# Kernel optimization log

Measured on AMD Instinct MI355X. Metric: run time of the kernel, lower is better.

Reference implementation:

```python
import jax, jax.numpy as jnp
import numpy as np

V = 32000   # vocab_size
H = 256     # hidden_dim
HALF = H // 2
B = 64
L = 2048
LN_EPS = 1e-5
DELTA_EPS = 1e-6


def setup_inputs() -> dict:
    key = jax.random.key(0)
    ks = jax.random.split(key, 8)
    s = 0.02
    return {
        "seq": jax.random.randint(ks[0], (B, L), 0, V),
        # Encoder params
        "embed": jax.random.normal(ks[1], (V, H), jnp.float32) * s,
        "W1": jax.random.normal(ks[2], (H, 2 * H), jnp.float32) * s,
        "b1": jnp.zeros((2 * H,), jnp.float32),
        "W2": jax.random.normal(ks[3], (2 * H, H), jnp.float32) * s,
        "b2": jnp.zeros((H,), jnp.float32),
        "gamma": jnp.ones((H,), jnp.float32),
        "beta": jnp.zeros((H,), jnp.float32),
        # sem_p: Linear(H, HALF)
        "Wp": jax.random.normal(ks[4], (H, HALF), jnp.float32) * s,
        "bp": jnp.zeros((HALF,), jnp.float32),
        # out: Linear(HALF, V)
        "Wo": jax.random.normal(ks[5], (HALF, V), jnp.float32) * s,
        "bo": jnp.zeros((V,), jnp.float32),
    }


def reference(seq, embed, W1, b1, W2, b2, gamma, beta, Wp, bp, Wo, bo):
    # Encoder: embed -> FFN -> residual -> LayerNorm
    e = embed[seq]                                      # [B, L, H]
    f = jnp.maximum(e @ W1 + b1, 0.0) @ W2 + b2         # [B, L, H]
    x = e + f
    mu = jnp.mean(x, axis=-1, keepdims=True)
    var = jnp.mean((x - mu) ** 2, axis=-1, keepdims=True)
    h = (x - mu) / jnp.sqrt(var + LN_EPS) * gamma + beta  # [B, L, H]

    # Project all timesteps once (sem_p applied to h[:, t] and the last query)
    p = h @ Wp + bp                                     # [B, L, HALF]

    # Delta-rule recurrent state update over t = 0 .. L-2
    ks_seq = jnp.swapaxes(p[:, :-1, :], 0, 1)           # [L-1, B, HALF]

    def step(M, k):
        vps = jnp.einsum('bij,bj->bi', M, k)            # read
        dvs = k - vps / (jnp.sum(k * k, axis=-1, keepdims=True) + DELTA_EPS)
        M = M + dvs[:, :, None] * k[:, None, :]         # rank-1 write
        return M, None

    M0 = jnp.zeros((B, HALF, HALF), h.dtype)
    M_s, _ = jax.lax.scan(step, M0, ks_seq)

    # Read with projected last-position query
    cs = jnp.einsum('bij,bj->bi', M_s, p[:, -1, :])     # [B, HALF]
    return cs @ Wo + bo                                 # [B, V]
```

## Files before the change

### kernel.cpp

```cpp
#include <hip/hip_runtime.h>

#define Vv 32000
#define Ll 2048

typedef __bf16 bf16x8 __attribute__((ext_vector_type(8)));
typedef float  f32x4  __attribute__((ext_vector_type(4)));

__device__ __forceinline__ unsigned short f2bf(float f) {
    unsigned u = __builtin_bit_cast(unsigned, f);
    u += 0x7fffu + ((u >> 16) & 1u);
    return (unsigned short)(u >> 16);
}
__device__ __forceinline__ float bf2f(unsigned short s) {
    unsigned u = (unsigned)s << 16;
    return __builtin_bit_cast(float, u);
}
__device__ __forceinline__ void unpk8(uint4 v, float* o) {
    o[0] = bf2f((unsigned short)(v.x & 0xffff)); o[1] = bf2f((unsigned short)(v.x >> 16));
    o[2] = bf2f((unsigned short)(v.y & 0xffff)); o[3] = bf2f((unsigned short)(v.y >> 16));
    o[4] = bf2f((unsigned short)(v.z & 0xffff)); o[5] = bf2f((unsigned short)(v.z >> 16));
    o[6] = bf2f((unsigned short)(v.w & 0xffff)); o[7] = bf2f((unsigned short)(v.w >> 16));
}

#define MFMA(a, b, c) __builtin_amdgcn_mfma_f32_16x16x32_bf16(a, b, c, 0, 0, 0)
#define GLL16(gsrc, ldst)                                                    \
    __builtin_amdgcn_global_load_lds(                                        \
        (const __attribute__((address_space(1))) void*)(gsrc),               \
        (__attribute__((address_space(3))) void*)(ldst), 16, 0, 0)
#define GLL4(gsrc, ldst)                                                     \
    __builtin_amdgcn_global_load_lds(                                        \
        (const __attribute__((address_space(1))) void*)(gsrc),               \
        (__attribute__((address_space(3))) void*)(ldst), 4, 0, 0)

__global__ __launch_bounds__(256) void prep_kernel(
    const float* __restrict__ W1, const float* __restrict__ W2,
    const float* __restrict__ Wp, unsigned short* __restrict__ W1T,
    unsigned short* __restrict__ W2T, unsigned short* __restrict__ WpT,
    float* __restrict__ zrow)
{
    int idx = blockIdx.x * 256 + threadIdx.x;
    if (blockIdx.x == 575 && threadIdx.x < 64) zrow[threadIdx.x] = 0.f;
    if (idx < 65536) {
        int e0 = idx * 2, n = e0 >> 8, k = e0 & 255;
        unsigned lo = f2bf(W1[(size_t)k * 512 + n]);
        unsigned hi = f2bf(W1[(size_t)(k + 1) * 512 + n]);
        ((unsigned*)W1T)[idx] = lo | (hi << 16);
    } else if (idx < 131072) {
        int i = idx - 65536, e0 = i * 2, n = e0 >> 9, k = e0 & 511;
        unsigned lo = f2bf(W2[(size_t)k * 256 + n]);
        unsigned hi = f2bf(W2[(size_t)(k + 1) * 256 + n]);
        ((unsigned*)W2T)[i] = lo | (hi << 16);
    } else {
        int i = idx - 131072, e0 = i * 2, n = e0 >> 8, k = e0 & 255;
        unsigned lo = f2bf(Wp[(size_t)k * 128 + n]);
        unsigned hi = f2bf(Wp[(size_t)(k + 1) * 128 + n]);
        ((unsigned*)WpT)[i] = lo | (hi << 16);
    }
}

__global__ __launch_bounds__(256) void embconv_kernel(
    const float* __restrict__ embed, unsigned short* __restrict__ embbf)
{
    int idx = blockIdx.x * 256 + threadIdx.x;
    const float4 a = ((const float4*)embed)[(size_t)idx * 2];
    const float4 b = ((const float4*)embed)[(size_t)idx * 2 + 1];
    uint4 pk;
    pk.x = (unsigned)f2bf(a.x) | ((unsigned)f2bf(a.y) << 16);
    pk.y = (unsigned)f2bf(a.z) | ((unsigned)f2bf(a.w) << 16);
    pk.z = (unsigned)f2bf(b.x) | ((unsigned)f2bf(b.y) << 16);
    pk.w = (unsigned)f2bf(b.z) | ((unsigned)f2bf(b.w) << 16);
    ((uint4*)embbf)[idx] = pk;
}

__global__ __launch_bounds__(512, 4) void enc_kernel(
    const unsigned short* __restrict__ embbf,
    const unsigned short* __restrict__ W1T, const float* __restrict__ b1,
    const unsigned short* __restrict__ W2T, const float* __restrict__ b2,
    const float* __restrict__ gamma, const float* __restrict__ beta,
    const unsigned short* __restrict__ WpT, const float* __restrict__ bp,
    unsigned short* __restrict__ ptab)
{
    __shared__ char sE[32 * 512];
    __shared__ char sU[32 * 1024];
    __shared__ float sPart[32][8][2];
    __shared__ float sMR[32][2];

    const int tid  = threadIdx.x;
    const int lane = tid & 63;
    const int w    = tid >> 6;
    const int l15  = lane & 15;
    const int lk   = lane >> 4;
    const int n0   = blockIdx.x * 32;
    const int swl  = (l15 & 7) << 4;

    #pragma unroll
    for (int cc = 0; cc < 2; ++cc) {
        int c = cc * 512 + tid;
        int row  = c >> 5;
        int slot = (c & 31) << 4;
        int kbs  = slot ^ ((row & 7) << 4);
        GLL16((const char*)embbf + (size_t)(n0 + row) * 512 + kbs,
              sE + (cc * 512 + (tid & 448)) * 16);
    }
    __syncthreads();

    #pragma unroll
    for (int nf2 = 0; nf2 < 2; ++nf2) {
        f32x4 acc1[2][2];
        acc1[0][0] = acc1[0][1] = acc1[1][0] = acc1[1][1] = (f32x4){0.f, 0.f, 0.f, 0.f};
        const char* w1p = (const char*)W1T + (size_t)(w * 64 + nf2 * 32 + l15) * 512 + lk * 16;
        bf16x8 bfr[16];
        #pragma unroll
        for (int ks = 0; ks < 8; ++ks) {
            bfr[ks * 2]     = *(const bf16x8*)(w1p + ks * 64);
            bfr[ks * 2 + 1] = *(const bf16x8*)(w1p + 16 * 512 + ks * 64);
        }
        #pragma unroll
        for (int ks = 0; ks < 8; ++ks) {
            int ka = (ks * 64 + lk * 16) ^ swl;
            bf16x8 a0 = *(const bf16x8*)(sE + l15 * 512 + ka);
            bf16x8 a1 = *(const bf16x8*)(sE + (16 + l15) * 512 + ka);
            acc1[0][0] = MFMA(a0, bfr[ks * 2],     acc1[0][0]);
            acc1[1][0] = MFMA(a1, bfr[ks * 2],     acc1[1][0]);
            acc1[0][1] = MFMA(a0, bfr[ks * 2 + 1], acc1[0][1]);
            acc1[1][1] = MFMA(a1, bfr[ks * 2 + 1], acc1[1][1]);
        }
        float bv0 = b1[w * 64 + nf2 * 32 + l15];
        float bv1 = b1[w * 64 + nf2 * 32 + 16 + l15];
        #pragma unroll
        for (int mi = 0; mi < 2; ++mi)
            #pragma unroll
            for (int nj = 0; nj < 2; ++nj) {
                float bv = nj ? bv1 : bv0;
                #pragma unroll
                for (int r = 0; r < 4; ++r) {
                    int row = mi * 16 + lk * 4 + r;
                    int col = w * 64 + nf2 * 32 + nj * 16 + l15;
                    float v = fmaxf(acc1[mi][nj][r] + bv, 0.f);
                    *(unsigned short*)(sU + row * 1024 + ((col * 2) ^ ((row & 7) << 4))) = f2bf(v);
                }
            }
    }
    __syncthreads();

    f32x4 acc2[2][2];
    acc2[0][0] = acc2[0][1] = acc2[1][0] = acc2[1][1] = (f32x4){0.f, 0.f, 0.f, 0.f};
    {
        const char* w2p = (const char*)W2T + (size_t)(w * 32 + l15) * 1024 + lk * 16;
        #pragma unroll
        for (int h = 0; h < 2; ++h) {
            bf16x8 bfr[16];
            #pragma unroll
            for (int ks = 0; ks < 8; ++ks) {
                int kss = h * 8 + ks;
                bfr[ks * 2]     = *(const bf16x8*)(w2p + kss * 64);
                bfr[ks * 2 + 1] = *(const bf16x8*)(w2p + 16 * 1024 + kss * 64);
            }
            #pragma unroll
            for (int ks = 0; ks < 8; ++ks) {
                int kss = h * 8 + ks;
                int ka = (kss * 64 + lk * 16) ^ swl;
                bf16x8 a0 = *(const bf16x8*)(sU + l15 * 1024 + ka);
                bf16x8 a1 = *(const bf16x8*)(sU + (16 + l15) * 1024 + ka);
                acc2[0][0] = MFMA(a0, bfr[ks * 2],     acc2[0][0]);
                acc2[1][0] = MFMA(a1, bfr[ks * 2],     acc2[1][0]);
                acc2[0][1] = MFMA(a0, bfr[ks * 2 + 1], acc2[0][1]);
                acc2[1][1] = MFMA(a1, bfr[ks * 2 + 1], acc2[1][1]);
            }
        }
    }

    float b2v[2], gv[2], btv[2];
    #pragma unroll
    for (int nj = 0; nj < 2; ++nj) {
        int col = w * 32 + nj * 16 + l15;
        b2v[nj] = b2[col]; gv[nj] = gamma[col]; btv[nj] = beta[col];
    }
    #pragma unroll
    for (int mi = 0; mi < 2; ++mi)
        #pragma unroll
        for (int r = 0; r < 4; ++r) {
            int row = mi * 16 + lk * 4 + r;
            int swr = (row & 7) << 4;
            float s1 = 0.f, s2 = 0.f;
            #pragma unroll
            for (int nj = 0; nj < 2; ++nj) {
                int col = w * 32 + nj * 16 + l15;
                float e = bf2f(*(const unsigned short*)(sE + row * 512 + ((col * 2) ^ swr)));
                float x = acc2[mi][nj][r] + b2v[nj] + e;
                acc2[mi][nj][r] = x;
                s1 += x; s2 = fmaf(x, x, s2);
            }
            s1 += __shfl_xor(s1, 1); s2 += __shfl_xor(s2, 1);
            s1 += __shfl_xor(s1, 2); s2 += __shfl_xor(s2, 2);
            s1 += __shfl_xor(s1, 4); s2 += __shfl_xor(s2, 4);
            s1 += __shfl_xor(s1, 8); s2 += __shfl_xor(s2, 8);
            if (l15 == 0) { sPart[row][w][0] = s1; sPart[row][w][1] = s2; }
        }
    __syncthreads();
    if (tid < 32) {
        float t1 = 0.f, t2 = 0.f;
        #pragma unroll
        for (int ww = 0; ww < 8; ++ww) { t1 += sPart[tid][ww][0]; t2 += sPart[tid][ww][1]; }
        float mu  = t1 * (1.f / 256.f);
        float var = t2 * (1.f / 256.f) - mu * mu;
        sMR[tid][0] = mu;
        sMR[tid][1] = rsqrtf(var + 1e-5f);
    }
    __syncthreads();
    #pragma unroll
    for (int mi = 0; mi < 2; ++mi)
        #pragma unroll
        for (int r = 0; r < 4; ++r) {
            int row = mi * 16 + lk * 4 + r;
            int swr = (row & 7) << 4;
            float mu = sMR[row][0], rs = sMR[row][1];
            #pragma unroll
            for (int nj = 0; nj < 2; ++nj) {
                int col = w * 32 + nj * 16 + l15;
                float h = (acc2[mi][nj][r] - mu) * rs * gv[nj] + btv[nj];
                *(unsigned short*)(sE + row * 512 + ((col * 2) ^ swr)) = f2bf(h);
            }
        }
    __syncthreads();

    f32x4 acc3[2];
    acc3[0] = acc3[1] = (f32x4){0.f, 0.f, 0.f, 0.f};
    {
        const char* wpp = (const char*)WpT + (size_t)(w * 16 + l15) * 512 + lk * 16;
        bf16x8 bfr[8];
        #pragma unroll
        for (int ks = 0; ks < 8; ++ks)
            bfr[ks] = *(const bf16x8*)(wpp + ks * 64);
        #pragma unroll
        for (int ks = 0; ks < 8; ++ks) {
            int ka = (ks * 64 + lk * 16) ^ swl;
            bf16x8 a0 = *(const bf16x8*)(sE + l15 * 512 + ka);
            bf16x8 a1 = *(const bf16x8*)(sE + (16 + l15) * 512 + ka);
            acc3[0] = MFMA(a0, bfr[ks], acc3[0]);
            acc3[1] = MFMA(a1, bfr[ks], acc3[1]);
        }
    }
    {
        float bpv = bp[w * 16 + l15];
        #pragma unroll
        for (int mi = 0; mi < 2; ++mi)
            #pragma unroll
            for (int r = 0; r < 4; ++r) {
                int row = mi * 16 + lk * 4 + r;
                int col = w * 16 + l15;
                *(unsigned short*)(sU + row * 256 + col * 2) = f2bf(acc3[mi][r] + bpv);
            }
    }
    __syncthreads();
    {
        int row = tid >> 4, slot = (tid & 15) << 4;
        *(uint4*)((char*)ptab + (size_t)(n0 + row) * 256 + slot) =
            *(const uint4*)(sU + row * 256 + slot);
    }
}

__global__ __launch_bounds__(256) void sprep_kernel(
    const int* __restrict__ seq, const unsigned short* __restrict__ ptab,
    char* __restrict__ SBg)
{
    __shared__ unsigned short sK[64 * 136];
    __shared__ float sG[10 * 16 * 17];
    __shared__ float sM[4 * 16 * 17];
    __shared__ float sQ[64];
    __shared__ float sW[64 * 132];

    const int blk  = blockIdx.x;
    const int b    = blk >> 5, ch = blk & 31;
    const int t_hi = 2047 - (ch << 6);
    const int tid  = threadIdx.x;
    const int lane = tid & 63;
    const int wv   = tid >> 6;
    const int l15  = lane & 15, lk = lane >> 4;

    #pragma unroll
    for (int i = 0; i < 4; ++i) {
        int c = i * 256 + tid;
        int row = c >> 4, j = c & 15;
        int t = t_hi - row;
        if (t == 2047) {
            *(uint4*)((char*)sK + row * 272 + j * 16) = (uint4){0u, 0u, 0u, 0u};
        } else {
            int v = seq[b * 2048 + t];
            *(uint4*)((char*)sK + row * 272 + j * 16) =
                *(const uint4*)((const char*)(ptab + (size_t)v * 128) + j * 16);
        }
    }
    __syncthreads();

    {
        int q = 0;
        #pragma unroll
        for (int ti = 0; ti < 4; ++ti)
            #pragma unroll
            for (int tj = 0; tj <= ti; ++tj, ++q) {
                if ((q & 3) != wv) continue;
                f32x4 acc = (f32x4){0.f, 0.f, 0.f, 0.f};
                #pragma unroll
                for (int ks = 0; ks < 4; ++ks) {
                    bf16x8 fa = *(const bf16x8*)((const char*)sK + (ti * 16 + l15) * 272 + ks * 64 + lk * 16);
                    bf16x8 fb = *(const bf16x8*)((const char*)sK + (tj * 16 + l15) * 272 + ks * 64 + lk * 16);
                    acc = MFMA(fa, fb, acc);
                }
                #pragma unroll
                for (int r = 0; r < 4; ++r)
                    sG[q * 272 + (lk * 4 + r) * 17 + l15] = acc[r];
            }
    }
    __syncthreads();

    if (tid < 64) {
        int dq = (lk * (lk + 3)) >> 1;
        float d = sG[dq * 272 + l15 * 17 + l15] + 1e-6f;
        sQ[tid] = 1.0f / d;
    }
    __syncthreads();

    if (tid < 64) {
        const int g = lk, c = l15;
        const float* Tg = &sG[((g * (g + 3)) >> 1) * 272];
        float qv[16], av[16], mcol[16];
        #pragma unroll
        for (int r = 0; r < 16; ++r) { qv[r] = sQ[g * 16 + r]; av[r] = 0.f; }
        #pragma unroll
        for (int r = 0; r < 16; ++r) {
            float mr = (((r == c) ? 1.f : 0.f) - av[r]) * qv[r];
            mcol[r] = mr;
            #pragma unroll
            for (int i = r + 1; i < 16; ++i)
                av[i] = fmaf(Tg[i * 17 + r], mr, av[i]);
        }
        #pragma unroll
        for (int r = 0; r < 16; ++r)
            sM[g * 272 + r * 17 + c] = mcol[r];
    }
    __syncthreads();

    const int rr = tid & 15, dq8 = tid >> 4;
    #pragma unroll 1
    for (int s = 0; s < 4; ++s) {
        float a[8];
        {
            uint4 kv = *(const uint4*)((const char*)sK + (16 * s + rr) * 272 + dq8 * 16);
            unpk8(kv, a);
        }
        #pragma unroll
        for (int j = 0; j < 3; ++j) {
            if (j >= s) break;
            const float* Tb = &sG[(((s * (s + 1)) >> 1) + j) * 272];
            #pragma unroll
            for (int m = 0; m < 16; ++m) {
                float t = Tb[rr * 17 + m];
                const float* wrow = &sW[(16 * j + m) * 132 + dq8 * 8];
                f32x4 w0 = *(const f32x4*)(wrow);
                f32x4 w1 = *(const f32x4*)(wrow + 4);
                a[0] = fmaf(-t, w0.x, a[0]); a[1] = fmaf(-t, w0.y, a[1]);
                a[2] = fmaf(-t, w0.z, a[2]); a[3] = fmaf(-t, w0.w, a[3]);
                a[4] = fmaf(-t, w1.x, a[4]); a[5] = fmaf(-t, w1.y, a[5]);
                a[6] = fmaf(-t, w1.z, a[6]); a[7] = fmaf(-t, w1.w, a[7]);
            }
        }
        {
            float* wrow = &sW[(16 * s + rr) * 132 + dq8 * 8];
            *(f32x4*)(wrow)     = (f32x4){a[0], a[1], a[2], a[3]};
            *(f32x4*)(wrow + 4) = (f32x4){a[4], a[5], a[6], a[7]};
        }
        __syncthreads();
        float o[8];
        #pragma unroll
        for (int v = 0; v < 8; ++v) o[v] = 0.f;
        #pragma unroll
        for (int cc = 0; cc < 16; ++cc) {
            float mm = sM[s * 272 + rr * 17 + cc];
            const float* wrow = &sW[(16 * s + cc) * 132 + dq8 * 8];
            f32x4 w0 = *(const f32x4*)(wrow);
            f32x4 w1 = *(const f32x4*)(wrow + 4);
            o[0] = fmaf(mm, w0.x, o[0]); o[1] = fmaf(mm, w0.y, o[1]);
            o[2] = fmaf(mm, w0.z, o[2]); o[3] = fmaf(mm, w0.w, o[3]);
            o[4] = fmaf(mm, w1.x, o[4]); o[5] = fmaf(mm, w1.y, o[5]);
            o[6] = fmaf(mm, w1.z, o[6]); o[7] = fmaf(mm, w1.w, o[7]);
        }
        __syncthreads();
        {
            float* wrow = &sW[(16 * s + rr) * 132 + dq8 * 8];
            *(f32x4*)(wrow)     = (f32x4){o[0], o[1], o[2], o[3]};
            *(f32x4*)(wrow + 4) = (f32x4){o[4], o[5], o[6], o[7]};
        }
        __syncthreads();
    }

    char* blob = SBg + (size_t)blk * 17408;
    unsigned* wtp = (unsigned*)blob;
    {
        int i = tid & 63;
        #pragma unroll
        for (int dg = 0; dg < 16; ++dg) {
            int d2 = (tid >> 6) * 16 + dg;
            float2 wvp = *(const float2*)&sW[i * 132 + d2 * 2];
            wtp[d2 * 64 + i] = (unsigned)f2bf(wvp.x) | ((unsigned)f2bf(wvp.y) << 16);
        }
    }
    if (tid < 64) {
        int dq = (lk * (lk + 3)) >> 1;
        float d = sG[dq * 272 + l15 * 17 + l15] + 1e-6f;
        *(float*)(blob + 16384 + tid * 4) = d;
    }
}

__global__ __launch_bounds__(512) void scan_kernel(
    const int* __restrict__ seq, const unsigned short* __restrict__ ptab,
    const char* __restrict__ SBg, const float* __restrict__ zrow,
    float* __restrict__ csb)
{
    __shared__ int sSeq[2048];
    __shared__ unsigned short sKb[2][8192];
    __shared__ __align__(16) char sBlob[2][16640];
    __shared__ float  sPZ[8][64];
    __shared__ float2 sPC[8][64];

    const int b    = blockIdx.x;
    const int tid  = threadIdx.x;
    const int lane = tid & 63;
    const int w    = tid >> 6;

    *(int4*)&sSeq[tid * 4] = *(const int4*)&seq[b * 2048 + tid * 4];
    float u0, u1;
    {
        int vq = seq[b * 2048 + 2047];
        unsigned pk = *(const unsigned*)(ptab + (size_t)vq * 128 + lane * 2);
        u0 = bf2f((unsigned short)(pk & 0xffff));
        u1 = bf2f((unsigned short)(pk >> 16));
    }
    float csv0 = 0.f, csv1 = 0.f;
    __syncthreads();

    auto STAGE = [&](int s, int ch) {
        int t_hi = 2047 - (ch << 6);
        #pragma unroll
        for (int kk = 0; kk < 2; ++kk) {
            int k = w * 2 + kk;
            int g = k * 64 + lane;
            int r = g >> 4, sd = g & 15;
            int t = t_hi - r;
            int v = sSeq[t];
            const char* srow = (t == 2047) ? (const char*)zrow
                                           : (const char*)(ptab + (size_t)v * 128);
            GLL16(srow + sd * 16, (char*)sKb[s] + k * 1024);
        }
        const char* bsrc = SBg + ((size_t)b * 32 + ch) * 17408;
        #pragma unroll
        for (int kk = 0; kk < 2; ++kk) {
            int k = w * 2 + kk;
            GLL16(bsrc + k * 1024 + lane * 16, (char*)sBlob[s] + k * 1024);
        }
        if (w == 7)
            GLL4(bsrc + 16384 + lane * 4, (char*)sBlob[s] + 16384);
    };

    STAGE(0, 0); STAGE(1, 1);

    #pragma unroll 1
    for (int c = 0; c < 32; ++c) {
        const int cur = c & 1;
        if (c < 31) {
            if (w == 7) asm volatile("s_waitcnt vmcnt(5)" ::: "memory");
            else        asm volatile("s_waitcnt vmcnt(4)" ::: "memory");
        } else {
            asm volatile("s_waitcnt vmcnt(0)" ::: "memory");
        }
        __builtin_amdgcn_s_barrier();
        __builtin_amdgcn_sched_barrier(0);

        const unsigned short* kb = sKb[cur];
        const unsigned* wt = (const unsigned*)(sBlob[cur]);
        const float* dgv = (const float*)(sBlob[cur] + 16384);

        float zp = 0.f;
        #pragma unroll
        for (int j = 0; j < 8; ++j) {
            int d2 = w * 8 + j;
            unsigned wp = wt[d2 * 64 + lane];
            float ua = __shfl(u0, d2);
            float ub = __shfl(u1, d2);
            zp = fmaf(bf2f((unsigned short)(wp & 0xffff)), ua, zp);
            zp = fmaf(bf2f((unsigned short)(wp >> 16)),    ub, zp);
        }
        sPZ[w][lane] = zp;
        asm volatile("s_waitcnt lgkmcnt(0)" ::: "memory");
        __builtin_amdgcn_s_barrier();
        __builtin_amdgcn_sched_barrier(0);

        float z = 0.f;
        #pragma unroll
        for (int ww = 0; ww < 8; ++ww) z += sPZ[ww][lane];
        float ci = z * dgv[lane];

        float du0 = 0.f, du1 = 0.f;
        #pragma unroll
        for (int j = 0; j < 8; ++j) {
            int i = w * 8 + j;
            float zi  = __shfl(z, i);
            float cii = __shfl(ci, i);
            unsigned kp = *(const unsigned*)((const char*)kb + i * 256 + lane * 4);
            float k0 = bf2f((unsigned short)(kp & 0xffff));
            float k1 = bf2f((unsigned short)(kp >> 16));
            du0  = fmaf(zi,  k0, du0);  du1  = fmaf(zi,  k1, du1);
            csv0 = fmaf(cii, k0, csv0); csv1 = fmaf(cii, k1, csv1);
        }
        sPC[w][lane] = make_float2(du0, du1);
        asm volatile("s_waitcnt lgkmcnt(0)" ::: "memory");
        __builtin_amdgcn_s_barrier();
        __builtin_amdgcn_sched_barrier(0);

        if (c + 2 < 32) STAGE(cur, c + 2);

        float s0 = 0.f, s1 = 0.f;
        #pragma unroll
        for (int ww = 0; ww < 8; ++ww) {
            float2 p = sPC[ww][lane];
            s0 += p.x; s1 += p.y;
        }
        u0 -= s0; u1 -= s1;
    }

    asm volatile("s_waitcnt lgkmcnt(0)" ::: "memory");
    __builtin_amdgcn_s_barrier();
    sPC[w][lane] = make_float2(csv0, csv1);
    asm volatile("s_waitcnt lgkmcnt(0)" ::: "memory");
    __builtin_amdgcn_s_barrier();
    if (w == 0) {
        float a0 = 0.f, a1 = 0.f;
        #pragma unroll
        for (int ww = 0; ww < 8; ++ww) {
            float2 p = sPC[ww][lane];
            a0 += p.x; a1 += p.y;
        }
        csb[b * 128 + lane * 2]     = a0;
        csb[b * 128 + lane * 2 + 1] = a1;
    }
}

__global__ __launch_bounds__(256) void out_kernel(
    const float* __restrict__ cs, const float* __restrict__ Wo,
    const float* __restrict__ bo, float* __restrict__ out)
{
    __shared__ float sC[64 * 128];
    const int tid = threadIdx.x;
    #pragma unroll
    for (int r = 0; r < 8; ++r)
        ((float4*)sC)[r * 256 + tid] = ((const float4*)cs)[r * 256 + tid];
    __syncthreads();

    const int j  = blockIdx.x * 64 + (tid & 63);
    const int rg = tid >> 6;
    float acc[16];
    #pragma unroll
    for (int r = 0; r < 16; ++r) acc[r] = 0.f;
    for (int k0 = 0; k0 < 128; k0 += 4) {
        float w0 = Wo[(size_t)(k0 + 0) * Vv + j];
        float w1 = Wo[(size_t)(k0 + 1) * Vv + j];
        float w2 = Wo[(size_t)(k0 + 2) * Vv + j];
        float w3 = Wo[(size_t)(k0 + 3) * Vv + j];
        #pragma unroll
        for (int r = 0; r < 16; ++r) {
            float4 c = *(const float4*)&sC[(rg * 16 + r) * 128 + k0];
            acc[r] = fmaf(c.x, w0, fmaf(c.y, w1, fmaf(c.z, w2, fmaf(c.w, w3, acc[r]))));
        }
    }
    float bj = bo[j];
    #pragma unroll
    for (int r = 0; r < 16; ++r)
        out[(size_t)(rg * 16 + r) * Vv + j] = acc[r] + bj;
}

extern "C" void kernel_launch(void* const* d_in, const int* in_sizes, int n_in,
                              void* d_out, int out_size, void* d_ws, size_t ws_size,
                              hipStream_t stream)
{
    const int*   seq   = (const int*)  d_in[0];
    const float* embed = (const float*)d_in[1];
    const float* W1    = (const float*)d_in[2];
    const float* b1    = (const float*)d_in[3];
    const float* W2    = (const float*)d_in[4];
    const float* b2    = (const float*)d_in[5];
    const float* gamma = (const float*)d_in[6];
    const float* beta  = (const float*)d_in[7];
    const float* Wp    = (const float*)d_in[8];
    const float* bp    = (const float*)d_in[9];
    const float* Wo    = (const float*)d_in[10];
    const float* bo    = (const float*)d_in[11];
    float* out = (float*)d_out;

    char* wsb = (char*)d_ws;
    unsigned short* ptab  = (unsigned short*)(wsb);
    char*           SBg   = wsb + 8192000;
    unsigned short* W1T   = (unsigned short*)(wsb + 43843584);
    unsigned short* W2T   = (unsigned short*)(wsb + 44105728);
    unsigned short* WpT   = (unsigned short*)(wsb + 44367872);
    float*          csb   = (float*)(wsb + 44433408);
    float*          zrow  = (float*)(wsb + 44466176);
    unsigned short* embbf = (unsigned short*)(wsb + 44466432);

    prep_kernel<<<576, 256, 0, stream>>>(W1, W2, Wp, W1T, W2T, WpT, zrow);
    embconv_kernel<<<4000, 256, 0, stream>>>(embed, embbf);
    enc_kernel<<<Vv / 32, 512, 0, stream>>>(embbf, W1T, b1, W2T, b2,
                                            gamma, beta, WpT, bp, ptab);
    sprep_kernel<<<2048, 256, 0, stream>>>(seq, ptab, SBg);
    scan_kernel<<<64, 512, 0, stream>>>(seq, ptab, SBg, zrow, csb);
    out_kernel<<<Vv / 64, 256, 0, stream>>>(csb, Wo, bo, out);
}
```

Measured before the change: 211.0 us.

## Split encoder into tiled FFN1 kernel and LDS-pipelined FFN2/projection kernel

The fused encoder kernel becomes two kernels. encA computes the first FFN layer with ReLU on 128x128 tiles, staging both the embeddings and W1 in shared memory, and writes the hidden activations to a global buffer. encB reloads those activations and streams W2 through a double-buffered shared-memory pipeline with explicit waitcnt and barriers. It also stages Wp in shared memory instead of loading it straight into registers. The aim is better weight reuse and less redundant global weight traffic per block, at the cost of a 32 MB intermediate write and read and one extra launch.

New measurement: 205.8 us. -2.5%, faster.

```diff
diff --git a/kernel.cpp b/kernel.cpp
--- a/kernel.cpp
+++ b/kernel.cpp
@@ -72,16 +72,95 @@
     ((uint4*)embbf)[idx] = pk;
 }
 
-__global__ __launch_bounds__(512, 4) void enc_kernel(
+__global__ __launch_bounds__(512, 2) void encA_kernel(
     const unsigned short* __restrict__ embbf,
     const unsigned short* __restrict__ W1T, const float* __restrict__ b1,
-    const unsigned short* __restrict__ W2T, const float* __restrict__ b2,
+    unsigned short* __restrict__ Ug)
+{
+    __shared__ char sA[65536];
+    __shared__ char sB[65536];
+
+    const int tid  = threadIdx.x;
+    const int lane = tid & 63;
+    const int w    = tid >> 6;
+    const int rh   = w >> 2;
+    const int cq   = w & 3;
+    const int l15  = lane & 15;
+    const int lk   = lane >> 4;
+    const int n0   = (blockIdx.x >> 2) * 128;
+    const int c0   = (blockIdx.x & 3) * 128;
+    const int swl  = (l15 & 7) << 4;
+
+    #pragma unroll
+    for (int i = 0; i < 8; ++i) {
+        int id = i * 512 + tid;
+        int row = id >> 5, slot = (id & 31) << 4;
+        GLL16((const char*)embbf + (size_t)(n0 + row) * 512 + (slot ^ ((row & 7) << 4)),
+              sA + (size_t)(i * 512 + (tid & 448)) * 16);
+    }
+    #pragma unroll
+    for (int i = 0; i < 8; ++i) {
+        int id = i * 512 + tid;
+        int col = id >> 5, slot = (id & 31) << 4;
+        GLL16((const char*)W1T + (size_t)(c0 + col) * 512 + (slot ^ ((col & 7) << 4)),
+              sB + (size_t)(i * 512 + (tid & 448)) * 16);
+    }
+    __syncthreads();
+
+    f32x4 acc[4][2];
+    #pragma unroll
+    for (int m = 0; m < 4; ++m)
+        #pragma unroll
+        for (int n = 0; n < 2; ++n) acc[m][n] = (f32x4){0.f, 0.f, 0.f, 0.f};
+    #pragma unroll
+    for (int ks = 0; ks < 8; ++ks) {
+        int ka = (ks * 64 + lk * 16) ^ swl;
+        bf16x8 b0 = *(const bf16x8*)(sB + (cq * 32 + l15) * 512 + ka);
+        bf16x8 b1v = *(const bf16x8*)(sB + (cq * 32 + 16 + l15) * 512 + ka);
+        #pragma unroll
+        for (int mi = 0; mi < 4; ++mi) {
+            bf16x8 a = *(const bf16x8*)(sA + (rh * 64 + mi * 16 + l15) * 512 + ka);
+            acc[mi][0] = MFMA(a, b0,  acc[mi][0]);
+            acc[mi][1] = MFMA(a, b1v, acc[mi][1]);
+        }
+    }
+
+    float bv0 = b1[c0 + cq * 32 + l15];
+    float bv1 = b1[c0 + cq * 32 + 16 + l15];
+    __syncthreads();
+    #pragma unroll
+    for (int mi = 0; mi < 4; ++mi)
+        #pragma unroll
+        for (int nj = 0; nj < 2; ++nj) {
+            float bv = nj ? bv1 : bv0;
+            #pragma unroll
+            for (int r = 0; r < 4; ++r) {
+                int row = rh * 64 + mi * 16 + lk * 4 + r;
+                int col = cq * 32 + nj * 16 + l15;
+                *(unsigned short*)(sA + row * 256 + col * 2) =
+                    f2bf(fmaxf(acc[mi][nj][r] + bv, 0.f));
+            }
+        }
+    __syncthreads();
+    #pragma unroll
+    for (int i = 0; i < 4; ++i) {
+        int id = i * 512 + tid;
+        int row = id >> 4, slot = (id & 15) << 4;
+        *(uint4*)((char*)Ug + (size_t)(n0 + row) * 1024 + c0 * 2 + slot) =
+            *(const uint4*)(sA + row * 256 + slot);
+    }
+}
+
+__global__ __launch_bounds__(512, 2) void encB_kernel(
+    const unsigned short* __restrict__ embbf, const unsigned short* __restrict__ Ug,
+    const char* __restrict__ W2Tc, const float* __restrict__ b2,
     const float* __restrict__ gamma, const float* __restrict__ beta,
     const unsigned short* __restrict__ WpT, const float* __restrict__ bp,
     unsigned short* __restrict__ ptab)
 {
     __shared__ char sE[32 * 512];
     __shared__ char sU[32 * 1024];
+    __shared__ char sWB[65536];
     __shared__ float sPart[32][8][2];
     __shared__ float sMR[32][2];
 
@@ -94,80 +173,69 @@
     const int swl  = (l15 & 7) << 4;
 
     #pragma unroll
-    for (int cc = 0; cc < 2; ++cc) {
-        int c = cc * 512 + tid;
-        int row  = c >> 5;
-        int slot = (c & 31) << 4;
-        int kbs  = slot ^ ((row & 7) << 4);
-        GLL16((const char*)embbf + (size_t)(n0 + row) * 512 + kbs,
-              sE + (cc * 512 + (tid & 448)) * 16);
-    }
-    __syncthreads();
-
-    #pragma unroll
-    for (int nf2 = 0; nf2 < 2; ++nf2) {
-        f32x4 acc1[2][2];
-        acc1[0][0] = acc1[0][1] = acc1[1][0] = acc1[1][1] = (f32x4){0.f, 0.f, 0.f, 0.f};
-        const char* w1p = (const char*)W1T + (size_t)(w * 64 + nf2 * 32 + l15) * 512 + lk * 16;
-        bf16x8 bfr[16];
-        #pragma unroll
-        for (int ks = 0; ks < 8; ++ks) {
-            bfr[ks * 2]     = *(const bf16x8*)(w1p + ks * 64);
-            bfr[ks * 2 + 1] = *(const bf16x8*)(w1p + 16 * 512 + ks * 64);
-        }
-        #pragma unroll
-        for (int ks = 0; ks < 8; ++ks) {
-            int ka = (ks * 64 + lk * 16) ^ swl;
-            bf16x8 a0 = *(const bf16x8*)(sE + l15 * 512 + ka);
-            bf16x8 a1 = *(const bf16x8*)(sE + (16 + l15) * 512 + ka);
-            acc1[0][0] = MFMA(a0, bfr[ks * 2],     acc1[0][0]);
-            acc1[1][0] = MFMA(a1, bfr[ks * 2],     acc1[1][0]);
-            acc1[0][1] = MFMA(a0, bfr[ks * 2 + 1], acc1[0][1]);
-            acc1[1][1] = MFMA(a1, bfr[ks * 2 + 1], acc1[1][1]);
-        }
-        float bv0 = b1[w * 64 + nf2 * 32 + l15];
-        float bv1 = b1[w * 64 + nf2 * 32 + 16 + l15];
-        #pragma unroll
-        for (int mi = 0; mi < 2; ++mi)
-            #pragma unroll
-            for (int nj = 0; nj < 2; ++nj) {
-                float bv = nj ? bv1 : bv0;
-                #pragma unroll
-                for (int r = 0; r < 4; ++r) {
-                    int row = mi * 16 + lk * 4 + r;
-                    int col = w * 64 + nf2 * 32 + nj * 16 + l15;
-                    float v = fmaxf(acc1[mi][nj][r] + bv, 0.f);
-                    *(unsigned short*)(sU + row * 1024 + ((col * 2) ^ ((row & 7) << 4))) = f2bf(v);
-                }
-            }
-    }
+    for (int i = 0; i < 2; ++i) {
+        int id = i * 512 + tid;
+        int row = id >> 5, slot = (id & 31) << 4;
+        GLL16((const char*)embbf + (size_t)(n0 + row) * 512 + (slot ^ ((row & 7) << 4)),
+              sE + (size_t)(i * 512 + (tid & 448)) * 16);
+    }
+    #pragma unroll
+    for (int i = 0; i < 4; ++i) {
+        int id = i * 512 + tid;
+        int row = id >> 6, slot = (id & 63) << 4;
+        GLL16((const char*)Ug + (size_t)(n0 + row) * 1024 + (slot ^ ((row & 7) << 4)),
+              sU + (size_t)(i * 512 + (tid & 448)) * 16);
+    }
+    auto STAGE_W = [&](int s, int kc) {
+        #pragma unroll
+        for (int i = 0; i < 4; ++i) {
+            int id = i * 512 + tid;
+            int col = id >> 3, j = id & 7;
+            GLL16(W2Tc + (size_t)col * 1024 + kc * 128 + ((j * 16) ^ ((col & 7) << 4)),
+                  sWB + s * 32768 + (size_t)(i * 512 + (tid & 448)) * 16);
+        }
+    };
+    STAGE_W(0, 0); STAGE_W(1, 1);
     __syncthreads();
 
     f32x4 acc2[2][2];
     acc2[0][0] = acc2[0][1] = acc2[1][0] = acc2[1][1] = (f32x4){0.f, 0.f, 0.f, 0.f};
-    {
-        const char* w2p = (const char*)W2T + (size_t)(w * 32 + l15) * 1024 + lk * 16;
-        #pragma unroll
-        for (int h = 0; h < 2; ++h) {
-            bf16x8 bfr[16];
-            #pragma unroll
-            for (int ks = 0; ks < 8; ++ks) {
-                int kss = h * 8 + ks;
-                bfr[ks * 2]     = *(const bf16x8*)(w2p + kss * 64);
-                bfr[ks * 2 + 1] = *(const bf16x8*)(w2p + 16 * 1024 + kss * 64);
-            }
-            #pragma unroll
-            for (int ks = 0; ks < 8; ++ks) {
-                int kss = h * 8 + ks;
-                int ka = (kss * 64 + lk * 16) ^ swl;
-                bf16x8 a0 = *(const bf16x8*)(sU + l15 * 1024 + ka);
-                bf16x8 a1 = *(const bf16x8*)(sU + (16 + l15) * 1024 + ka);
-                acc2[0][0] = MFMA(a0, bfr[ks * 2],     acc2[0][0]);
-                acc2[1][0] = MFMA(a1, bfr[ks * 2],     acc2[1][0]);
-                acc2[0][1] = MFMA(a0, bfr[ks * 2 + 1], acc2[0][1]);
-                acc2[1][1] = MFMA(a1, bfr[ks * 2 + 1], acc2[1][1]);
-            }
-        }
+    #pragma unroll 1
+    for (int c = 0; c < 8; ++c) {
+        const int cur = c & 1;
+        if (c >= 2) {
+            if (c < 7) { asm volatile("s_waitcnt vmcnt(4)" ::: "memory"); }
+            else       { asm volatile("s_waitcnt vmcnt(0)" ::: "memory"); }
+        }
+        __builtin_amdgcn_s_barrier();
+        __builtin_amdgcn_sched_barrier(0);
+
+        const char* wb = sWB + cur * 32768;
+        #pragma unroll
+        for (int ks2 = 0; ks2 < 2; ++ks2) {
+            int kwb = (ks2 * 64 + lk * 16) ^ swl;
+            int kau = (c * 128 + ks2 * 64 + lk * 16) ^ swl;
+            bf16x8 b0  = *(const bf16x8*)(wb + (w * 32 + l15) * 128 + kwb);
+            bf16x8 b1v = *(const bf16x8*)(wb + (w * 32 + 16 + l15) * 128 + kwb);
+            bf16x8 a0  = *(const bf16x8*)(sU + l15 * 1024 + kau);
+            bf16x8 a1  = *(const bf16x8*)(sU + (16 + l15) * 1024 + kau);
+            acc2[0][0] = MFMA(a0, b0,  acc2[0][0]);
+            acc2[1][0] = MFMA(a1, b0,  acc2[1][0]);
+            acc2[0][1] = MFMA(a0, b1v, acc2[0][1]);
+            acc2[1][1] = MFMA(a1, b1v, acc2[1][1]);
+        }
+        asm volatile("s_waitcnt lgkmcnt(0)" ::: "memory");
+        __builtin_amdgcn_s_barrier();
+        __builtin_amdgcn_sched_barrier(0);
+        if (c + 2 < 8) STAGE_W(cur, c + 2);
+    }
+
+    #pragma unroll
+    for (int i = 0; i < 8; ++i) {
+        int id = i * 512 + tid;
+        int col = id >> 5, slot = (id & 31) << 4;
+        GLL16((const char*)WpT + (size_t)col * 512 + (slot ^ ((col & 7) << 4)),
+              sWB + (size_t)(i * 512 + (tid & 448)) * 16);
     }
 
     float b2v[2], gv[2], btv[2];
@@ -226,20 +294,14 @@
 
     f32x4 acc3[2];
     acc3[0] = acc3[1] = (f32x4){0.f, 0.f, 0.f, 0.f};
-    {
-        const char* wpp = (const char*)WpT + (size_t)(w * 16 + l15) * 512 + lk * 16;
-        bf16x8 bfr[8];
-        #pragma unroll
-        for (int ks = 0; ks < 8; ++ks)
-            bfr[ks] = *(const bf16x8*)(wpp + ks * 64);
-        #pragma unroll
-        for (int ks = 0; ks < 8; ++ks) {
-            int ka = (ks * 64 + lk * 16) ^ swl;
-            bf16x8 a0 = *(const bf16x8*)(sE + l15 * 512 + ka);
-            bf16x8 a1 = *(const bf16x8*)(sE + (16 + l15) * 512 + ka);
-            acc3[0] = MFMA(a0, bfr[ks], acc3[0]);
-            acc3[1] = MFMA(a1, bfr[ks], acc3[1]);
-        }
+    #pragma unroll
+    for (int ks = 0; ks < 8; ++ks) {
+        int ka = (ks * 64 + lk * 16) ^ swl;
+        bf16x8 b0 = *(const bf16x8*)(sWB + (w * 16 + l15) * 512 + ka);
+        bf16x8 a0 = *(const bf16x8*)(sE + l15 * 512 + ka);
+        bf16x8 a1 = *(const bf16x8*)(sE + (16 + l15) * 512 + ka);
+        acc3[0] = MFMA(a0, b0, acc3[0]);
+        acc3[1] = MFMA(a1, b0, acc3[1]);
     }
     {
         float bpv = bp[w * 16 + l15];
@@ -599,17 +661,19 @@
     char* wsb = (char*)d_ws;
     unsigned short* ptab  = (unsigned short*)(wsb);
     char*           SBg   = wsb + 8192000;
-    unsigned short* W1T   = (unsigned short*)(wsb + 43843584);
-    unsigned short* W2T   = (unsigned short*)(wsb + 44105728);
-    unsigned short* WpT   = (unsigned short*)(wsb + 44367872);
-    float*          csb   = (float*)(wsb + 44433408);
-    float*          zrow  = (float*)(wsb + 44466176);
-    unsigned short* embbf = (unsigned short*)(wsb + 44466432);
+    unsigned short* embbf = (unsigned short*)(wsb + 8192000);
+    unsigned short* Ug    = (unsigned short*)(wsb + 24576000);
+    unsigned short* W1T   = (unsigned short*)(wsb + 57344000);
+    unsigned short* W2T   = (unsigned short*)(wsb + 57606144);
+    unsigned short* WpT   = (unsigned short*)(wsb + 57868288);
+    float*          csb   = (float*)(wsb + 57933824);
+    float*          zrow  = (float*)(wsb + 57966592);
 
     prep_kernel<<<576, 256, 0, stream>>>(W1, W2, Wp, W1T, W2T, WpT, zrow);
     embconv_kernel<<<4000, 256, 0, stream>>>(embed, embbf);
-    enc_kernel<<<Vv / 32, 512, 0, stream>>>(embbf, W1T, b1, W2T, b2,
-                                            gamma, beta, WpT, bp, ptab);
+    encA_kernel<<<1000, 512, 0, stream>>>(embbf, W1T, b1, Ug);
+    encB_kernel<<<1000, 512, 0, stream>>>(embbf, Ug, (const char*)W2T, b2,
+                                          gamma, beta, WpT, bp, ptab);
     sprep_kernel<<<2048, 256, 0, stream>>>(seq, ptab, SBg);
     scan_kernel<<<64, 512, 0, stream>>>(seq, ptab, SBg, zrow, csb);
     out_kernel<<<Vv / 64, 256, 0, stream>>>(csb, Wo, bo, out);
```
